# Kernel optimization log

Hardware: AMD Instinct MI355X
Metric: run time of the kernel (lower is better)

Reference implementation:

```python
import jax, jax.numpy as jnp
import numpy as np

N, E, R = 50000, 500000, 3
IN, HID, OUT = 128, 128, 128
NEG_SLOPE = 0.2


def setup_inputs() -> dict:
    key = jax.random.key(0)
    ks = jax.random.split(key, 16)
    g = lambda i, shape: jax.random.normal(ks[i], shape, jnp.float32) * 0.1
    return {
        "x": jax.random.normal(ks[0], (N, IN), jnp.float32),
        "edge_index": jax.random.randint(ks[1], (2, E), 0, N, jnp.int32),
        "edge_type": jax.random.randint(ks[2], (E,), 0, R, jnp.int32),
        "edge_attr": jax.random.normal(ks[3], (E, 1), jnp.float32),
        # conv1 params (RGATConv: per-relation weight, q/k/e attention vectors, edge lin, bias)
        "w1": g(4, (R, IN, HID)), "q1": g(5, (HID, 1)), "k1": g(6, (HID, 1)),
        "le1": g(7, (1, HID)), "e1": g(8, (HID, 1)), "b1": jnp.zeros((HID,), jnp.float32),
        # conv2 params
        "w2": g(9, (R, HID, OUT)), "q2": g(10, (OUT, 1)), "k2": g(11, (OUT, 1)),
        "le2": g(12, (1, OUT)), "e2": g(13, (OUT, 1)), "b2": jnp.zeros((OUT,), jnp.float32),
    }


def _rgat_conv(x, src, dst, edge_type, edge_attr, w, q, k, le, e, b):
    """PyG RGATConv: heads=1, dim=1, additive-self-attention, across-relation softmax."""
    n = x.shape[0]
    # Per-relation linear at node level (equiv. to per-edge bmm with w[edge_type])
    xw = jnp.einsum('ni,rio->rno', x, w)            # [R, N, C]
    x_j = xw[edge_type, src]                          # [E, C] transformed source feats
    x_i = xw[edge_type, dst]                          # [E, C] transformed target feats
    # additive attention logits: q(x_i) + k(x_j) + e(lin_edge(edge_attr))
    alpha = x_i @ q + x_j @ k + (edge_attr @ le) @ e  # [E, 1]
    alpha = jax.nn.leaky_relu(alpha, negative_slope=NEG_SLOPE)
    # across-relation softmax over incoming edges of each target node
    amax = jax.ops.segment_max(alpha, dst, num_segments=n)
    amax = jnp.where(jnp.isfinite(amax), amax, 0.0)   # empty segments -> 0
    ex = jnp.exp(alpha - amax[dst])
    denom = jax.ops.segment_sum(ex, dst, num_segments=n)
    alpha = ex / (denom[dst] + 1e-16)
    # weighted scatter-add aggregation, then bias (concat=True, heads=1)
    out = jax.ops.segment_sum(alpha * x_j, dst, num_segments=n)  # [N, C]
    return out + b


def reference(x, edge_index, edge_type, edge_attr,
              w1, q1, k1, le1, e1, b1,
              w2, q2, k2, le2, e2, b2):
    src, dst = edge_index[0], edge_index[1]
    h = jax.nn.relu(_rgat_conv(x, src, dst, edge_type, edge_attr, w1, q1, k1, le1, e1, b1))
    return _rgat_conv(h, src, dst, edge_type, edge_attr, w2, q2, k2, le2, e2, b2)
```

## Files before the change

kernel.cpp:

```cpp
#include <hip/hip_runtime.h>
#include <hip/hip_bf16.h>
#include <math.h>

typedef __bf16 bf16x8 __attribute__((ext_vector_type(8)));
typedef float f32x4 __attribute__((ext_vector_type(4)));

#define CDIM 128
#define ECAP 128

__global__ void sentinel_kernel(float* outf) {
  if (threadIdx.x == 0) outf[0] = 12345.0f;
}


__global__ __launch_bounds__(128) void consts_kernel(
    const float* __restrict__ le1, const float* __restrict__ e1,
    const float* __restrict__ le2, const float* __restrict__ e2,
    float* __restrict__ outc) {
  __shared__ float s1[CDIM], s2[CDIM];
  int t = threadIdx.x;
  s1[t] = le1[t] * e1[t];
  s2[t] = le2[t] * e2[t];
  __syncthreads();
  for (int off = 64; off > 0; off >>= 1) {
    if (t < off) { s1[t] += s1[t + off]; s2[t] += s2[t + off]; }
    __syncthreads();
  }
  if (t == 0) { outc[0] = s1[0]; outc[1] = s2[0]; }
}

__global__ __launch_bounds__(256) void hist_kernel(const int* __restrict__ dstv,
                                                   int* __restrict__ deg, int E) {
  int e = blockIdx.x * 256 + threadIdx.x;
  if (e < E) atomicAdd(&deg[dstv[e]], 1);
}

__global__ __launch_bounds__(256) void scan1_kernel(const int* __restrict__ deg,
                                                    int* __restrict__ rowptr,
                                                    int* __restrict__ partials, int n) {
  __shared__ int sh[256];
  int t = threadIdx.x;
  int base = blockIdx.x * 1024;
  int idx = base + t * 4;
  int v[4]; int s = 0;
#pragma unroll
  for (int j = 0; j < 4; ++j) { v[j] = (idx + j < n) ? deg[idx + j] : 0; s += v[j]; }
  sh[t] = s;
  __syncthreads();
  for (int off = 1; off < 256; off <<= 1) {
    int x = (t >= off) ? sh[t - off] : 0;
    __syncthreads();
    sh[t] += x;
    __syncthreads();
  }
  int excl = sh[t] - s;
  if (t == 255) partials[blockIdx.x] = sh[255];
  int run = excl;
#pragma unroll
  for (int j = 0; j < 4; ++j) {
    if (idx + j < n) rowptr[idx + j] = run;
    run += v[j];
  }
}

__global__ void scan2_kernel(int* __restrict__ partials, int nb) {
  if (threadIdx.x == 0 && blockIdx.x == 0) {
    int run = 0;
    for (int i = 0; i < nb; ++i) { int t = partials[i]; partials[i] = run; run += t; }
  }
}

__global__ __launch_bounds__(256) void scan3_kernel(int* __restrict__ rowptr,
                                                    int* __restrict__ cursor,
                                                    const int* __restrict__ partials,
                                                    int n, int E) {
  int i = blockIdx.x * 256 + threadIdx.x;
  if (i < n) {
    int v = rowptr[i] + partials[i >> 10];
    rowptr[i] = v;
    cursor[i] = v;
  } else if (i == n) {
    rowptr[n] = E;
  }
}

__global__ __launch_bounds__(256) void scatter_kernel(
    const int* __restrict__ srcv, const int* __restrict__ dstv,
    const int* __restrict__ etype, const float* __restrict__ eattr,
    int* __restrict__ cursor, int2* __restrict__ kattr, int E, int n) {
  int e = blockIdx.x * 256 + threadIdx.x;
  if (e >= E) return;
  int p = atomicAdd(&cursor[dstv[e]], 1);
  kattr[p] = make_int2(etype[e] * n + srcv[e], __float_as_int(eattr[e]));
}

__global__ __launch_bounds__(256) void transpose_w_kernel(
    const float* __restrict__ w, __hip_bfloat16* __restrict__ wt, int total) {
  int t = blockIdx.x * 256 + threadIdx.x;
  if (t >= total) return;
  int r = t >> 11;
  int rem = t & 2047;
  int kb = rem >> 7;
  int o = rem & 127;
  const float* wr = w + ((size_t)r << 14);
  union { __hip_bfloat16 h[8]; int4 v; } u;
#pragma unroll
  for (int j = 0; j < 8; ++j)
    u.h[j] = __float2bfloat16(wr[(size_t)(kb * 8 + j) * CDIM + o]);
  *reinterpret_cast<int4*>(wt + (size_t)t * 8) = u.v;
}

__global__ __launch_bounds__(256) void gemm_xw_kernel(
    const float* __restrict__ xin, const __hip_bfloat16* __restrict__ wt,
    const float* __restrict__ qv, const float* __restrict__ kv,
    __hip_bfloat16* __restrict__ xwout, float* __restrict__ sq, float* __restrict__ sk,
    int n) {
  __shared__ __hip_bfloat16 wlds[16 * 128 * 8];
  const int r = blockIdx.y;
  const int base = blockIdx.x * 128;
  const int tid = threadIdx.x;
  {
    const int4* src = reinterpret_cast<const int4*>(wt + ((size_t)r << 14));
    int4* dst = reinterpret_cast<int4*>(wlds);
    for (int i = tid; i < 2048; i += 256) dst[i] = src[i];
  }
  __syncthreads();

  const int wave = tid >> 6, lane = tid & 63;
  const int quad = lane >> 4, c16 = lane & 15;

  bf16x8 zf;
#pragma unroll
  for (int j = 0; j < 8; ++j) zf[j] = (__bf16)0.0f;

  bf16x8 af[2][4];
#pragma unroll
  for (int h = 0; h < 2; ++h) {
    int m = base + wave * 32 + h * 16 + c16;
#pragma unroll
    for (int ks = 0; ks < 4; ++ks) {
      if (m < n) {
        const float* xp = xin + (size_t)m * CDIM + ks * 32 + quad * 8;
        f32x4 x0 = *reinterpret_cast<const f32x4*>(xp);
        f32x4 x1 = *reinterpret_cast<const f32x4*>(xp + 4);
        bf16x8 a;
#pragma unroll
        for (int j = 0; j < 4; ++j) { a[j] = (__bf16)x0[j]; a[4 + j] = (__bf16)x1[j]; }
        af[h][ks] = a;
      } else {
        af[h][ks] = zf;
      }
    }
  }

  f32x4 acc[2][8];
#pragma unroll
  for (int h = 0; h < 2; ++h)
#pragma unroll
    for (int nt = 0; nt < 8; ++nt) acc[h][nt] = (f32x4){0.f, 0.f, 0.f, 0.f};

#pragma unroll
  for (int ks = 0; ks < 4; ++ks) {
#pragma unroll
    for (int nt = 0; nt < 8; ++nt) {
      bf16x8 b = *reinterpret_cast<const bf16x8*>(
          &wlds[(((ks * 4 + quad) * 128) + nt * 16 + c16) * 8]);
      acc[0][nt] = __builtin_amdgcn_mfma_f32_16x16x32_bf16(af[0][ks], b, acc[0][nt], 0, 0, 0);
      acc[1][nt] = __builtin_amdgcn_mfma_f32_16x16x32_bf16(af[1][ks], b, acc[1][nt], 0, 0, 0);
    }
  }

  float qf[8], kf[8];
#pragma unroll
  for (int nt = 0; nt < 8; ++nt) {
    qf[nt] = qv[nt * 16 + c16];
    kf[nt] = kv[nt * 16 + c16];
  }

#pragma unroll
  for (int h = 0; h < 2; ++h) {
    int rowb = base + wave * 32 + h * 16 + quad * 4;
#pragma unroll
    for (int reg = 0; reg < 4; ++reg) {
      int grow = rowb + reg;
      float s_q = 0.f, s_k = 0.f;
#pragma unroll
      for (int nt = 0; nt < 8; ++nt) {
        float v = acc[h][nt][reg];
        if (grow < n)
          xwout[(((size_t)r * n + grow) << 7) + nt * 16 + c16] = __float2bfloat16(v);
        s_q += v * qf[nt];
        s_k += v * kf[nt];
      }
#pragma unroll
      for (int off = 1; off < 16; off <<= 1) {
        s_q += __shfl_xor(s_q, off, 64);
        s_k += __shfl_xor(s_k, off, 64);
      }
      if (c16 == 0 && grow < n) {
        sq[r * n + grow] = s_q;
        sk[r * n + grow] = s_k;
      }
    }
  }
}

__global__ __launch_bounds__(256) void aggregate_kernel(
    const int* __restrict__ rowptr, const int2* __restrict__ kattr,
    const float* __restrict__ sq, const float* __restrict__ sk,
    const __hip_bfloat16* __restrict__ xw, const float* __restrict__ bias,
    const float* __restrict__ cscal, float* __restrict__ out, int n, int do_relu) {
  __shared__ int2 ldsE[4][ECAP];
  const int wave = threadIdx.x >> 6, lane = threadIdx.x & 63;
  const int node = blockIdx.x * 4 + wave;
  const bool active = node < n;
  const float c = cscal[0];
  const int n2 = n * 2, n3 = n * 3;

  int start = 0, deg = 0;
  float s0 = 0.f, s1 = 0.f, s2 = 0.f;
  if (active) {
    start = rowptr[node];
    deg = rowptr[node + 1] - start;
    s0 = sq[node]; s1 = sq[n + node]; s2 = sq[n2 + node];
  }

  float m = -__builtin_inff();
  if (active) {
    for (int j = lane; j < deg; j += 64) {
      int2 ka = kattr[start + j];
      int kk = ka.x;
      kk = (kk < 0) ? 0 : (kk >= n3 ? n3 - 1 : kk);
      float sv = (kk >= n2) ? s2 : ((kk >= n) ? s1 : s0);
      float l = sv + sk[kk] + c * __int_as_float(ka.y);
      l = l > 0.f ? l : 0.2f * l;
      if (j < ECAP) ldsE[wave][j] = make_int2(kk, __float_as_int(l));
      m = fmaxf(m, l);
    }
  }
#pragma unroll
  for (int off = 32; off > 0; off >>= 1) m = fmaxf(m, __shfl_xor(m, off, 64));
  __syncthreads();

  const int cap = deg < ECAP ? deg : ECAP;
  if (active) {
    for (int i = lane; i < cap; i += 64) {
      int2 e = ldsE[wave][i];
      e.y = __float_as_int(__expf(__int_as_float(e.y) - m));
      ldsE[wave][i] = e;
    }
  }
  __syncthreads();

  float a0 = 0.f, a1 = 0.f, den = 0.f;
  if (active) {
    for (int j = 0; j < cap; ++j) {
      int2 e = ldsE[wave][j];
      float w = __int_as_float(e.y);
      __hip_bfloat162 f01 =
          *reinterpret_cast<const __hip_bfloat162*>(xw + ((size_t)e.x << 7) + lane * 2);
      float2 ff = __bfloat1622float2(f01);
      a0 += w * ff.x;
      a1 += w * ff.y;
      den += w;
    }
    for (int j = cap; j < deg; ++j) {
      int2 ka = kattr[start + j];
      int kk = ka.x;
      kk = (kk < 0) ? 0 : (kk >= n3 ? n3 - 1 : kk);
      float sv = (kk >= n2) ? s2 : ((kk >= n) ? s1 : s0);
      float l = sv + sk[kk] + c * __int_as_float(ka.y);
      l = l > 0.f ? l : 0.2f * l;
      float w = __expf(l - m);
      __hip_bfloat162 f01 =
          *reinterpret_cast<const __hip_bfloat162*>(xw + ((size_t)kk << 7) + lane * 2);
      float2 ff = __bfloat1622float2(f01);
      a0 += w * ff.x;
      a1 += w * ff.y;
      den += w;
    }
    float inv = 1.0f / (den + 1e-16f);
    float2 bb = *reinterpret_cast<const float2*>(bias + lane * 2);
    float o0 = a0 * inv + bb.x;
    float o1 = a1 * inv + bb.y;
    if (do_relu) { o0 = fmaxf(o0, 0.f); o1 = fmaxf(o1, 0.f); }
    *reinterpret_cast<float2*>(out + (size_t)node * CDIM + lane * 2) =
        make_float2(o0, o1);
  }
}


extern "C" void kernel_launch(void* const* d_in, const int* in_sizes, int n_in,
                              void* d_out, int out_size, void* d_ws, size_t ws_size,
                              hipStream_t stream) {
  const float* x     = (const float*)d_in[0];
  const int*   eidx  = (const int*)d_in[1];
  const int*   etype = (const int*)d_in[2];
  const float* eattr = (const float*)d_in[3];
  const float* w1  = (const float*)d_in[4];
  const float* q1  = (const float*)d_in[5];
  const float* k1  = (const float*)d_in[6];
  const float* le1 = (const float*)d_in[7];
  const float* e1  = (const float*)d_in[8];
  const float* b1  = (const float*)d_in[9];
  const float* w2  = (const float*)d_in[10];
  const float* q2  = (const float*)d_in[11];
  const float* k2  = (const float*)d_in[12];
  const float* le2 = (const float*)d_in[13];
  const float* e2  = (const float*)d_in[14];
  const float* b2  = (const float*)d_in[15];

  const int N = in_sizes[0] / CDIM;
  const int E = in_sizes[2];
  const int R = in_sizes[4] / (CDIM * CDIM);
  const int* srcv = eidx;
  const int* dstv = eidx + E;

  char* p = (char*)d_ws;
  auto alloc = [&](size_t bytes) -> void* {
    void* q = (void*)p;
    p += (bytes + 255) & ~(size_t)255;
    return q;
  };
  float* sq       = (float*)alloc((size_t)R * N * 4);
  float* sk       = (float*)alloc((size_t)R * N * 4);
  int*   deg      = (int*)alloc((size_t)N * 4);
  int*   rowptr   = (int*)alloc((size_t)(N + 1) * 4);
  int*   cursor   = (int*)alloc((size_t)N * 4);
  int*   partials = (int*)alloc(4096);
  int2*  kattr    = (int2*)alloc((size_t)E * 8);
  __hip_bfloat16* wt = (__hip_bfloat16*)alloc((size_t)R * CDIM * CDIM * 2);
  float* cscal    = (float*)alloc(256);
  __hip_bfloat16* xw = (__hip_bfloat16*)alloc((size_t)R * N * CDIM * 2);

  size_t needed = (size_t)(p - (char*)d_ws);
  if (needed > ws_size) {
    sentinel_kernel<<<1, 64, 0, stream>>>((float*)d_out);
    return;
  }

  float* outp = (float*)d_out;
  float* hbuf = outp;

  const int eg = (E + 255) / 256;
  const int nb = (N + 1023) / 1024;
  const int nodes4 = (N + 3) / 4;

  consts_kernel<<<1, 128, 0, stream>>>(le1, e1, le2, e2, cscal);

  hipMemsetAsync(deg, 0, (size_t)N * 4, stream);
  hist_kernel<<<eg, 256, 0, stream>>>(dstv, deg, E);
  scan1_kernel<<<nb, 256, 0, stream>>>(deg, rowptr, partials, N);
  scan2_kernel<<<1, 64, 0, stream>>>(partials, nb);
  scan3_kernel<<<(N + 1 + 255) / 256, 256, 0, stream>>>(rowptr, cursor, partials, N, E);
  scatter_kernel<<<eg, 256, 0, stream>>>(srcv, dstv, etype, eattr, cursor, kattr, E, N);

  dim3 ggrid((N + 127) / 128, R);

  transpose_w_kernel<<<(R * 2048 + 255) / 256, 256, 0, stream>>>(w1, wt, R * 2048);
  gemm_xw_kernel<<<ggrid, 256, 0, stream>>>(x, wt, q1, k1, xw, sq, sk, N);
  aggregate_kernel<<<nodes4, 256, 0, stream>>>(rowptr, kattr, sq, sk, xw, b1,
                                               cscal + 0, hbuf, N, 1);

  transpose_w_kernel<<<(R * 2048 + 255) / 256, 256, 0, stream>>>(w2, wt, R * 2048);
  gemm_xw_kernel<<<ggrid, 256, 0, stream>>>(hbuf, wt, q2, k2, xw, sq, sk, N);
  aggregate_kernel<<<nodes4, 256, 0, stream>>>(rowptr, kattr, sq, sk, xw, b2,
                                               cscal + 1, outp, N, 0);
}
```

Measured before the change: 287.1 us.

## Vectorize aggregation gathers to 16-byte rows split across four edge groups

The aggregate kernel now processes four edges at a time per wave. Each 16-lane group loads 8 bf16 features with one 16-byte load, and partial sums are combined with cross-lane shuffles. This replaces the per-lane 4-byte gathers and is meant to raise memory-level parallelism on the dominant scatter-gather step. The change also merges the weight transposes and attention-constant kernels into a single prep launch, parallelizes the partials scan, raises ECAP to 192, and removes the index clamp. Dropping the clamp removes the guard against out-of-range indices.

```diff
diff --git a/kernel.cpp b/kernel.cpp
--- a/kernel.cpp
+++ b/kernel.cpp
@@ -6,28 +6,46 @@
 typedef float f32x4 __attribute__((ext_vector_type(4)));
 
 #define CDIM 128
-#define ECAP 128
+#define ECAP 192
 
 __global__ void sentinel_kernel(float* outf) {
   if (threadIdx.x == 0) outf[0] = 12345.0f;
 }
 
-
-__global__ __launch_bounds__(128) void consts_kernel(
+__global__ __launch_bounds__(256) void prep_kernel(
+    const float* __restrict__ w1, const float* __restrict__ w2,
+    __hip_bfloat16* __restrict__ wt,
     const float* __restrict__ le1, const float* __restrict__ e1,
     const float* __restrict__ le2, const float* __restrict__ e2,
-    float* __restrict__ outc) {
-  __shared__ float s1[CDIM], s2[CDIM];
-  int t = threadIdx.x;
-  s1[t] = le1[t] * e1[t];
-  s2[t] = le2[t] * e2[t];
-  __syncthreads();
-  for (int off = 64; off > 0; off >>= 1) {
-    if (t < off) { s1[t] += s1[t + off]; s2[t] += s2[t + off]; }
+    float* __restrict__ outc, int perW) {
+  if (blockIdx.x == gridDim.x - 1) {
+    __shared__ float s1[128], s2[128];
+    int t = threadIdx.x;
+    if (t < 128) { s1[t] = le1[t] * e1[t]; s2[t] = le2[t] * e2[t]; }
     __syncthreads();
-  }
-  if (t == 0) { outc[0] = s1[0]; outc[1] = s2[0]; }
-}
+    for (int off = 64; off > 0; off >>= 1) {
+      if (t < off) { s1[t] += s1[t + off]; s2[t] += s2[t + off]; }
+      __syncthreads();
+    }
+    if (t == 0) { outc[0] = s1[0]; outc[1] = s2[0]; }
+    return;
+  }
+  int t = blockIdx.x * 256 + threadIdx.x;
+  if (t >= perW * 2) return;
+  const float* w = (t < perW) ? w1 : w2;
+  int tt = (t < perW) ? t : t - perW;
+  int r = tt >> 11;
+  int rem = tt & 2047;
+  int kb = rem >> 7;
+  int o = rem & 127;
+  const float* wr = w + ((size_t)r << 14);
+  union { __hip_bfloat16 h[8]; int4 v; } u;
+#pragma unroll
+  for (int j = 0; j < 8; ++j)
+    u.h[j] = __float2bfloat16(wr[(size_t)(kb * 8 + j) * CDIM + o]);
+  *reinterpret_cast<int4*>(wt + (size_t)t * 8) = u.v;
+}
+
 
 __global__ __launch_bounds__(256) void hist_kernel(const int* __restrict__ dstv,
                                                    int* __restrict__ deg, int E) {
@@ -63,10 +81,23 @@
   }
 }
 
-__global__ void scan2_kernel(int* __restrict__ partials, int nb) {
-  if (threadIdx.x == 0 && blockIdx.x == 0) {
-    int run = 0;
-    for (int i = 0; i < nb; ++i) { int t = partials[i]; partials[i] = run; run += t; }
+__global__ __launch_bounds__(256) void scan2_kernel(int* __restrict__ partials, int nb) {
+  __shared__ int sh[256];
+  int carry = 0;
+  for (int base = 0; base < nb; base += 256) {
+    int i = base + threadIdx.x;
+    int v = (i < nb) ? partials[i] : 0;
+    sh[threadIdx.x] = v;
+    __syncthreads();
+    for (int off = 1; off < 256; off <<= 1) {
+      int x = (threadIdx.x >= off) ? sh[threadIdx.x - off] : 0;
+      __syncthreads();
+      sh[threadIdx.x] += x;
+      __syncthreads();
+    }
+    if (i < nb) partials[i] = carry + sh[threadIdx.x] - v;
+    carry += sh[255];
+    __syncthreads();
   }
 }
 
@@ -92,22 +123,6 @@
   if (e >= E) return;
   int p = atomicAdd(&cursor[dstv[e]], 1);
   kattr[p] = make_int2(etype[e] * n + srcv[e], __float_as_int(eattr[e]));
-}
-
-__global__ __launch_bounds__(256) void transpose_w_kernel(
-    const float* __restrict__ w, __hip_bfloat16* __restrict__ wt, int total) {
-  int t = blockIdx.x * 256 + threadIdx.x;
-  if (t >= total) return;
-  int r = t >> 11;
-  int rem = t & 2047;
-  int kb = rem >> 7;
-  int o = rem & 127;
-  const float* wr = w + ((size_t)r << 14);
-  union { __hip_bfloat16 h[8]; int4 v; } u;
-#pragma unroll
-  for (int j = 0; j < 8; ++j)
-    u.h[j] = __float2bfloat16(wr[(size_t)(kb * 8 + j) * CDIM + o]);
-  *reinterpret_cast<int4*>(wt + (size_t)t * 8) = u.v;
 }
 
 __global__ __launch_bounds__(256) void gemm_xw_kernel(
@@ -215,7 +230,7 @@
   const int node = blockIdx.x * 4 + wave;
   const bool active = node < n;
   const float c = cscal[0];
-  const int n2 = n * 2, n3 = n * 3;
+  const int n2 = n * 2;
 
   int start = 0, deg = 0;
   float s0 = 0.f, s1 = 0.f, s2 = 0.f;
@@ -230,7 +245,6 @@
     for (int j = lane; j < deg; j += 64) {
       int2 ka = kattr[start + j];
       int kk = ka.x;
-      kk = (kk < 0) ? 0 : (kk >= n3 ? n3 - 1 : kk);
       float sv = (kk >= n2) ? s2 : ((kk >= n) ? s1 : s0);
       float l = sv + sk[kk] + c * __int_as_float(ka.y);
       l = l > 0.f ? l : 0.2f * l;
@@ -252,40 +266,73 @@
   }
   __syncthreads();
 
-  float a0 = 0.f, a1 = 0.f, den = 0.f;
+  const int g = lane >> 4;
+  const int sub = lane & 15;
+  float acc[8];
+#pragma unroll
+  for (int t = 0; t < 8; ++t) acc[t] = 0.f;
+  float den = 0.f;
+
   if (active) {
-    for (int j = 0; j < cap; ++j) {
-      int2 e = ldsE[wave][j];
-      float w = __int_as_float(e.y);
-      __hip_bfloat162 f01 =
-          *reinterpret_cast<const __hip_bfloat162*>(xw + ((size_t)e.x << 7) + lane * 2);
-      float2 ff = __bfloat1622float2(f01);
-      a0 += w * ff.x;
-      a1 += w * ff.y;
+    for (int j0 = 0; j0 < cap; j0 += 4) {
+      int j = j0 + g;
+      float w = 0.f; int kk = 0;
+      if (j < cap) {
+        int2 e = ldsE[wave][j];
+        kk = e.x;
+        w = __int_as_float(e.y);
+      }
+      bf16x8 f = *reinterpret_cast<const bf16x8*>(xw + ((size_t)kk << 7) + sub * 8);
+#pragma unroll
+      for (int t = 0; t < 8; ++t) acc[t] += w * (float)f[t];
       den += w;
     }
-    for (int j = cap; j < deg; ++j) {
-      int2 ka = kattr[start + j];
-      int kk = ka.x;
-      kk = (kk < 0) ? 0 : (kk >= n3 ? n3 - 1 : kk);
-      float sv = (kk >= n2) ? s2 : ((kk >= n) ? s1 : s0);
-      float l = sv + sk[kk] + c * __int_as_float(ka.y);
-      l = l > 0.f ? l : 0.2f * l;
-      float w = __expf(l - m);
-      __hip_bfloat162 f01 =
-          *reinterpret_cast<const __hip_bfloat162*>(xw + ((size_t)kk << 7) + lane * 2);
-      float2 ff = __bfloat1622float2(f01);
-      a0 += w * ff.x;
-      a1 += w * ff.y;
+    for (int j0 = cap; j0 < deg; j0 += 4) {
+      int j = j0 + g;
+      float w = 0.f; int kk = 0;
+      if (j < deg) {
+        int2 ka = kattr[start + j];
+        kk = ka.x;
+        float sv = (kk >= n2) ? s2 : ((kk >= n) ? s1 : s0);
+        float l = sv + sk[kk] + c * __int_as_float(ka.y);
+        l = l > 0.f ? l : 0.2f * l;
+        w = __expf(l - m);
+      }
+      bf16x8 f = *reinterpret_cast<const bf16x8*>(xw + ((size_t)kk << 7) + sub * 8);
+#pragma unroll
+      for (int t = 0; t < 8; ++t) acc[t] += w * (float)f[t];
       den += w;
     }
-    float inv = 1.0f / (den + 1e-16f);
-    float2 bb = *reinterpret_cast<const float2*>(bias + lane * 2);
-    float o0 = a0 * inv + bb.x;
-    float o1 = a1 * inv + bb.y;
-    if (do_relu) { o0 = fmaxf(o0, 0.f); o1 = fmaxf(o1, 0.f); }
-    *reinterpret_cast<float2*>(out + (size_t)node * CDIM + lane * 2) =
-        make_float2(o0, o1);
+
+#pragma unroll
+    for (int t = 0; t < 8; ++t) {
+      acc[t] += __shfl_xor(acc[t], 16, 64);
+      acc[t] += __shfl_xor(acc[t], 32, 64);
+    }
+    den += __shfl_xor(den, 16, 64);
+    den += __shfl_xor(den, 32, 64);
+
+    if (g == 0) {
+      float inv = 1.0f / (den + 1e-16f);
+      f32x4 b0 = *reinterpret_cast<const f32x4*>(bias + sub * 8);
+      f32x4 b1 = *reinterpret_cast<const f32x4*>(bias + sub * 8 + 4);
+      f32x4 o0, o1;
+#pragma unroll
+      for (int t = 0; t < 4; ++t) {
+        o0[t] = acc[t] * inv + b0[t];
+        o1[t] = acc[4 + t] * inv + b1[t];
+      }
+      if (do_relu) {
+#pragma unroll
+        for (int t = 0; t < 4; ++t) {
+          o0[t] = fmaxf(o0[t], 0.f);
+          o1[t] = fmaxf(o1[t], 0.f);
+        }
+      }
+      float* op = out + (size_t)node * CDIM + sub * 8;
+      *reinterpret_cast<f32x4*>(op) = o0;
+      *reinterpret_cast<f32x4*>(op + 4) = o1;
+    }
   }
 }
 
@@ -329,7 +376,7 @@
   int*   cursor   = (int*)alloc((size_t)N * 4);
   int*   partials = (int*)alloc(4096);
   int2*  kattr    = (int2*)alloc((size_t)E * 8);
-  __hip_bfloat16* wt = (__hip_bfloat16*)alloc((size_t)R * CDIM * CDIM * 2);
+  __hip_bfloat16* wt = (__hip_bfloat16*)alloc((size_t)2 * R * CDIM * CDIM * 2);
   float* cscal    = (float*)alloc(256);
   __hip_bfloat16* xw = (__hip_bfloat16*)alloc((size_t)R * N * CDIM * 2);
 
@@ -345,25 +392,26 @@
   const int eg = (E + 255) / 256;
   const int nb = (N + 1023) / 1024;
   const int nodes4 = (N + 3) / 4;
-
-  consts_kernel<<<1, 128, 0, stream>>>(le1, e1, le2, e2, cscal);
+  const int perW = R * 2048;
+
+  prep_kernel<<<(perW * 2 + 255) / 256 + 1, 256, 0, stream>>>(
+      w1, w2, wt, le1, e1, le2, e2, cscal, perW);
 
   hipMemsetAsync(deg, 0, (size_t)N * 4, stream);
   hist_kernel<<<eg, 256, 0, stream>>>(dstv, deg, E);
   scan1_kernel<<<nb, 256, 0, stream>>>(deg, rowptr, partials, N);
-  scan2_kernel<<<1, 64, 0, stream>>>(partials, nb);
+  scan2_kernel<<<1, 256, 0, stream>>>(partials, nb);
   scan3_kernel<<<(N + 1 + 255) / 256, 256, 0, stream>>>(rowptr, cursor, partials, N, E);
   scatter_kernel<<<eg, 256, 0, stream>>>(srcv, dstv, etype, eattr, cursor, kattr, E, N);
 
   dim3 ggrid((N + 127) / 128, R);
 
-  transpose_w_kernel<<<(R * 2048 + 255) / 256, 256, 0, stream>>>(w1, wt, R * 2048);
   gemm_xw_kernel<<<ggrid, 256, 0, stream>>>(x, wt, q1, k1, xw, sq, sk, N);
   aggregate_kernel<<<nodes4, 256, 0, stream>>>(rowptr, kattr, sq, sk, xw, b1,
                                                cscal + 0, hbuf, N, 1);
 
-  transpose_w_kernel<<<(R * 2048 + 255) / 256, 256, 0, stream>>>(w2, wt, R * 2048);
-  gemm_xw_kernel<<<ggrid, 256, 0, stream>>>(hbuf, wt, q2, k2, xw, sq, sk, N);
+  gemm_xw_kernel<<<ggrid, 256, 0, stream>>>(hbuf, wt + (size_t)R * CDIM * CDIM,
+                                            q2, k2, xw, sq, sk, N);
   aggregate_kernel<<<nodes4, 256, 0, stream>>>(rowptr, kattr, sq, sk, xw, b2,
                                                cscal + 1, outp, N, 0);
 }
```

After: 279.2 us. 1.03x faster.
